# Performance work log

Hardware: AMD Instinct MI355X
Metric: run time of the kernel (lower is better)

## Reference

```python
import jax, jax.numpy as jnp
import numpy as np

N = 50000
E = 1600000
IN_C = 165
HID = 256
HEADS = 8
OUT_C = 2
NEG_SLOPE = 0.2


def setup_inputs() -> dict:
    key = jax.random.key(0)
    ks = jax.random.split(key, 10)
    x = jax.random.normal(ks[0], (N, IN_C), dtype=jnp.float32)
    edge_index = jax.random.randint(ks[1], (2, E), 0, N, dtype=jnp.int64)
    c1 = HID // HEADS  # 32 per-head channels in layer 1
    W1 = jax.random.normal(ks[2], (IN_C, HEADS * c1), dtype=jnp.float32) * (1.0 / np.sqrt(IN_C))
    att_src1 = jax.random.normal(ks[3], (HEADS, c1), dtype=jnp.float32) * 0.1
    att_dst1 = jax.random.normal(ks[4], (HEADS, c1), dtype=jnp.float32) * 0.1
    b1 = jnp.zeros((HEADS * c1,), dtype=jnp.float32)
    W2 = jax.random.normal(ks[5], (HID, 1 * OUT_C), dtype=jnp.float32) * (1.0 / np.sqrt(HID))
    att_src2 = jax.random.normal(ks[6], (1, OUT_C), dtype=jnp.float32) * 0.1
    att_dst2 = jax.random.normal(ks[7], (1, OUT_C), dtype=jnp.float32) * 0.1
    b2 = jnp.zeros((OUT_C,), dtype=jnp.float32)
    return {"x": x, "edge_index": edge_index, "W1": W1, "att_src1": att_src1,
            "att_dst1": att_dst1, "b1": b1, "W2": W2, "att_src2": att_src2,
            "att_dst2": att_dst2, "b2": b2}


def _gat_conv(x, src, dst, W, att_src, att_dst, bias, heads, concat):
    """PyG GATConv (eval mode, self-loops already appended to src/dst)."""
    n = x.shape[0]
    c = att_src.shape[1]
    h = (x @ W).reshape(n, heads, c)                      # [N, H, C]
    a_src = jnp.einsum('nhc,hc->nh', h, att_src)          # [N, H]
    a_dst = jnp.einsum('nhc,hc->nh', h, att_dst)
    e = a_src[src] + a_dst[dst]                           # [Et, H]
    e = jax.nn.leaky_relu(e, NEG_SLOPE)
    # segment softmax over incoming edges of each dst node
    e_max = jax.ops.segment_max(e, dst, num_segments=n)   # [N, H]
    e_exp = jnp.exp(e - e_max[dst])
    denom = jax.ops.segment_sum(e_exp, dst, num_segments=n)
    alpha = e_exp / denom[dst]                            # [Et, H]
    msg = alpha[:, :, None] * h[src]                      # [Et, H, C]
    out = jax.ops.segment_sum(msg, dst, num_segments=n)   # [N, H, C]
    if concat:
        out = out.reshape(n, heads * c)
    else:
        out = out.mean(axis=1)
    return out + bias


def reference(x, edge_index, W1, att_src1, att_dst1, b1, W2, att_src2, att_dst2, b2):
    n = x.shape[0]
    loops = jnp.arange(n, dtype=edge_index.dtype)
    src = jnp.concatenate([edge_index[0], loops])  # add_self_loops=True (PyG default)
    dst = jnp.concatenate([edge_index[1], loops])
    h = _gat_conv(x, src, dst, W1, att_src1, att_dst1, b1, HEADS, True)
    h = jax.nn.elu(h)
    out = _gat_conv(h, src, dst, W2, att_src2, att_dst2, b2, 1, False)
    return out
```

## Files before the change

### kernel.cpp

```cpp
#include <hip/hip_runtime.h>
#include <hip/hip_bf16.h>
#include <math.h>

#define N_NODES 50000
#define N_EDGES 1600000
#define IN_C 165
#define HID 256
#define HEADS 8
#define C1 32
#define OUT_C 2
#define NEG_SLOPE 0.2f
#define LOG2E 1.44269504088896f
#define TROWS 32
#define GEMM_BLOCKS ((N_NODES + TROWS - 1) / TROWS)
#define SCB 2048
#define SGRP 256
#define NPP ((N_NODES + 7) / 8)
#define CAPL 96
#define NE4 (N_EDGES / 4)

#define NSTEP 11
#define BIMG_BYTES ((size_t)NSTEP * 16384)
#define WAIMG_BYTES ((size_t)NSTEP * 2048)
#define WT (NSTEP * 512)
#define WPB ((WT + 255) / 256)
#define WAT (176 * 16)
#define WAB ((WAT + 255) / 256)

typedef float f32x2 __attribute__((ext_vector_type(2)));
typedef short s16x8 __attribute__((ext_vector_type(8)));
typedef float f32x16 __attribute__((ext_vector_type(16)));

__device__ inline float lrelu(float v) { return v > 0.f ? v : NEG_SLOPE * v; }
__device__ inline float e2l(float t) { return exp2f(fmaxf(t, NEG_SLOPE * t)); }

__device__ inline unsigned short f32_bf16(float f) {
    unsigned u = __float_as_uint(f);
    return (unsigned short)((u + 0x7FFFu + ((u >> 16) & 1u)) >> 16);
}

__device__ inline float bflo(unsigned u) { return __uint_as_float(u << 16); }
__device__ inline float bfhi(unsigned u) { return __uint_as_float(u & 0xFFFF0000u); }
__device__ inline float bf2f(unsigned short b) { return __uint_as_float(((unsigned)b) << 16); }

__global__ __launch_bounds__(256) void prep_kernel(
        const float* __restrict__ W,
        const float* __restrict__ att_src, const float* __restrict__ att_dst,
        unsigned short* __restrict__ bImg, unsigned short* __restrict__ waImg) {
    if (blockIdx.x < WPB) {
        int g2 = blockIdx.x * 256 + threadIdx.x;
        if (g2 >= WT) return;
        int s = g2 >> 9;
        int r9 = g2 & 511;
        int kg = r9 >> 8, nsub = (r9 >> 5) & 7, c32 = r9 & 31;
        int col = nsub * 32 + c32;
        int k0 = s * 16 + kg * 8;
        unsigned short hb[8], lb[8];
        #pragma unroll
        for (int i = 0; i < 8; ++i) {
            int k = k0 + i;
            float v = (k < IN_C) ? W[(size_t)k * HID + col] : 0.f;
            hb[i] = f32_bf16(v);
            lb[i] = f32_bf16(v - bf2f(hb[i]));
        }
        unsigned ph[4], pl[4];
        #pragma unroll
        for (int q = 0; q < 4; ++q) {
            ph[q] = (unsigned)hb[2*q] | ((unsigned)hb[2*q+1] << 16);
            pl[q] = (unsigned)lb[2*q] | ((unsigned)lb[2*q+1] << 16);
        }
        unsigned short* base = bImg + (size_t)s * 8192
                             + ((nsub * 2 + kg) * 32 + c32) * 8;
        *(uint4*)(base)        = make_uint4(ph[0], ph[1], ph[2], ph[3]);
        *(uint4*)(base + 4096) = make_uint4(pl[0], pl[1], pl[2], pl[3]);
    } else {
        int g2 = (blockIdx.x - WPB) * 256 + threadIdx.x;
        if (g2 >= WAT) return;
        int k = g2 >> 4, j = g2 & 15;
        int head = j >> 1;
        float dotv = 0.f;
        if (k < IN_C) {
            const float* wr = W + (size_t)k * HID + head * 32;
            const float* at = ((j & 1) ? att_dst : att_src) + head * 32;
            #pragma unroll
            for (int c = 0; c < 32; c += 4) {
                float4 wv = *(const float4*)(wr + c);
                float4 av = *(const float4*)(at + c);
                dotv += wv.x*av.x + wv.y*av.y + wv.z*av.z + wv.w*av.w;
            }
        }
        unsigned short dh = f32_bf16(dotv);
        unsigned short dl = f32_bf16(dotv - bf2f(dh));
        int s = k >> 4, kk = k & 15, kg = kk >> 3, i = kk & 7;
        unsigned short* base = waImg + (size_t)s * 1024 + (kg * 32 + j) * 8 + i;
        base[0]   = dh;
        base[512] = dl;
    }
}

__device__ __forceinline__ void gemm_mfma_block(
        int b, const float* __restrict__ x,
        const unsigned short* __restrict__ bImg,
        const unsigned short* __restrict__ waImg,
        unsigned short* __restrict__ h, float* __restrict__ a_src,
        float* __restrict__ a_dst, unsigned short* asr) {
    const int tid = threadIdx.x;
    const int w = tid >> 6, l = tid & 63;
    const int half = l >> 5, ln = l & 31;
    const int row0 = b * TROWS;
    for (int g = tid; g < 704; g += 256) {
        int o = g >> 5, row = g & 31;
        int s = o >> 1, kg = o & 1;
        int node = row0 + row;
        int k0 = o * 8;
        unsigned short hb[8], lb[8];
        #pragma unroll
        for (int i = 0; i < 8; ++i) {
            int k = k0 + i;
            float v = (node < N_NODES && k < IN_C) ? x[(size_t)node * IN_C + k] : 0.f;
            hb[i] = f32_bf16(v);
            lb[i] = f32_bf16(v - bf2f(hb[i]));
        }
        unsigned ph[4], pl[4];
        #pragma unroll
        for (int q = 0; q < 4; ++q) {
            ph[q] = (unsigned)hb[2*q] | ((unsigned)hb[2*q+1] << 16);
            pl[q] = (unsigned)lb[2*q] | ((unsigned)lb[2*q+1] << 16);
        }
        unsigned short* base = asr + s * 1024 + (kg * 32 + row) * 8;
        *(uint4*)(base)       = make_uint4(ph[0], ph[1], ph[2], ph[3]);
        *(uint4*)(base + 512) = make_uint4(pl[0], pl[1], pl[2], pl[3]);
    }
    __syncthreads();

    f32x16 acc0, acc1, accA;
    #pragma unroll
    for (int r = 0; r < 16; ++r) { acc0[r] = 0.f; acc1[r] = 0.f; accA[r] = 0.f; }
    const int ns0 = 2 * w, ns1 = 2 * w + 1;
    const int afo = (half * 32 + ln) * 8;
    const int fo0 = ((ns0 * 2 + half) * 32 + ln) * 8;
    const int fo1 = ((ns1 * 2 + half) * 32 + ln) * 8;
    for (int s = 0; s < NSTEP; ++s) {
        const unsigned short* ab = asr + s * 1024;
        s16x8 a_h = *(const s16x8*)(ab + afo);
        s16x8 a_l = *(const s16x8*)(ab + 512 + afo);
        const unsigned short* bb = bImg + (size_t)s * 8192;
        s16x8 bh0 = *(const s16x8*)(bb + fo0);
        s16x8 bh1 = *(const s16x8*)(bb + fo1);
        s16x8 bl0 = *(const s16x8*)(bb + 4096 + fo0);
        s16x8 bl1 = *(const s16x8*)(bb + 4096 + fo1);
        acc0 = __builtin_amdgcn_mfma_f32_32x32x16_bf16(a_h, bh0, acc0, 0, 0, 0);
        acc1 = __builtin_amdgcn_mfma_f32_32x32x16_bf16(a_h, bh1, acc1, 0, 0, 0);
        acc0 = __builtin_amdgcn_mfma_f32_32x32x16_bf16(a_h, bl0, acc0, 0, 0, 0);
        acc1 = __builtin_amdgcn_mfma_f32_32x32x16_bf16(a_h, bl1, acc1, 0, 0, 0);
        acc0 = __builtin_amdgcn_mfma_f32_32x32x16_bf16(a_l, bh0, acc0, 0, 0, 0);
        acc1 = __builtin_amdgcn_mfma_f32_32x32x16_bf16(a_l, bh1, acc1, 0, 0, 0);
        if (w == 0) {
            const unsigned short* wb = waImg + (size_t)s * 1024;
            s16x8 wah = *(const s16x8*)(wb + afo);
            s16x8 wal = *(const s16x8*)(wb + 512 + afo);
            accA = __builtin_amdgcn_mfma_f32_32x32x16_bf16(a_h, wah, accA, 0, 0, 0);
            accA = __builtin_amdgcn_mfma_f32_32x32x16_bf16(a_h, wal, accA, 0, 0, 0);
            accA = __builtin_amdgcn_mfma_f32_32x32x16_bf16(a_l, wah, accA, 0, 0, 0);
        }
    }
    #pragma unroll
    for (int t = 0; t < 2; ++t) {
        const int colg = w * 64 + t * 32 + ln;
        #pragma unroll
        for (int r = 0; r < 16; ++r) {
            int row = (r & 3) + 8 * (r >> 2) + 4 * half;
            int gr = row0 + row;
            if (gr < N_NODES) {
                float a = t ? acc1[r] : acc0[r];
                h[(size_t)gr * HID + colg] = f32_bf16(a);
            }
        }
    }
    if (w == 0 && ln < 16) {
        int head = ln >> 1;
        float* ap = (ln & 1) ? a_dst : a_src;
        #pragma unroll
        for (int r = 0; r < 16; ++r) {
            int row = (r & 3) + 8 * (r >> 2) + 4 * half;
            int gr = row0 + row;
            if (gr < N_NODES) ap[gr * 8 + head] = accA[r] * LOG2E;
        }
    }
}

__global__ __launch_bounds__(256) void fusedAB_kernel(
        const float* __restrict__ x,
        const unsigned short* __restrict__ bImg,
        const unsigned short* __restrict__ waImg,
        unsigned short* __restrict__ h, float* __restrict__ a_src,
        float* __restrict__ a_dst,
        const int* __restrict__ src, const int* __restrict__ dst,
        int* __restrict__ deg, unsigned short* __restrict__ csr) {
    __shared__ unsigned short asr[NSTEP * 1024];
    if (blockIdx.x < GEMM_BLOCKS) {
        gemm_mfma_block(blockIdx.x, x, bImg, waImg, h, a_src, a_dst, asr);
    } else {
        const int sb  = blockIdx.x - GEMM_BLOCKS;
        const int cls = sb & 7;
        const int blk = sb >> 3;
        const int lo = cls * NPP;
        const int hi = (lo + NPP < N_NODES) ? lo + NPP : N_NODES;
        const int t = blk * 256 + threadIdx.x;
        const int4* dst4 = (const int4*)dst;
        for (int uu = t; uu < NE4; uu += SGRP * 256) {
            int4 dv = dst4[uu];
            #pragma unroll
            for (int j = 0; j < 4; ++j) {
                int d = (j == 0) ? dv.x : (j == 1) ? dv.y : (j == 2) ? dv.z : dv.w;
                if (d >= lo && d < hi) {
                    int slot = atomicAdd(&deg[d], 1);
                    csr[(size_t)d * CAPL + slot] = (unsigned short)src[4 * uu + j];
                }
            }
        }
    }
}

__global__ __launch_bounds__(256) void agg1_fused_kernel(
        const int* __restrict__ deg, const unsigned short* __restrict__ csr,
        const float* __restrict__ a_src, const float* __restrict__ a_dst,
        const unsigned short* __restrict__ h1, const float* __restrict__ bias1,
        const float* __restrict__ W2,
        const float* __restrict__ as2, const float* __restrict__ ad2,
        float4* __restrict__ pk, float* __restrict__ a2d) {
    int wid = (blockIdx.x * 256 + threadIdx.x) >> 6;
    int l = threadIdx.x & 63;
    if (wid >= N_NODES) return;
    const int el = l >> 5;
    const int q  = l & 31;
    const int hd = q >> 2;
    const int ch = q * 8;
    const int sh = el * 16;
    const uint4* lst4 = (const uint4*)(csr + (size_t)wid * CAPL);
    const int n = deg[wid];
    const float ad_p = a_dst[wid * 8 + hd];
    float den = 0.f;
    f32x2 ac0 = {0.f, 0.f}, ac1 = {0.f, 0.f}, ac2 = {0.f, 0.f}, ac3 = {0.f, 0.f};

    uint4 ca = lst4[0], cb = lst4[1], cc = lst4[2], cd = lst4[3];
    int i = 0;

#define EXTRACT_S(S_, MK_, OFF_, W0_, W1_, W2_, W3_, W4_, W5_, W6_, W7_)      \
    {                                                                          \
        unsigned wsel_[8] = {W0_, W1_, W2_, W3_, W4_, W5_, W6_, W7_};          \
        _Pragma("unroll")                                                      \
        for (int j = 0; j < 8; ++j) {                                          \
            int sv = (int)((wsel_[j] >> sh) & 0xFFFFu);                        \
            int e = i + OFF_ + 2 * j + el;                                     \
            bool ok = e < n;                                                   \
            MK_[j] = ok ? 1.f : 0.f;                                           \
            S_[j] = ok ? sv : wid;                                             \
        }                                                                      \
    }

#define GATHER_ACC(S_, MK_, CNT_)                                              \
    {                                                                          \
        uint4 v_[CNT_];                                                        \
        _Pragma("unroll")                                                      \
        for (int j = 0; j < CNT_; ++j)                                         \
            v_[j] = *(const uint4*)(h1 + (size_t)S_[j] * HID + ch);            \
        float w_[CNT_];                                                        \
        _Pragma("unroll")                                                      \
        for (int j = 0; j < CNT_; ++j)                                         \
            w_[j] = MK_[j] * e2l(a_src[S_[j] * 8 + hd] + ad_p);                \
        _Pragma("unroll")                                                      \
        for (int j = 0; j < CNT_; ++j) {                                       \
            den += w_[j];                                                      \
            f32x2 w2_ = {w_[j], w_[j]};                                        \
            ac0 += w2_ * (f32x2){bflo(v_[j].x), bfhi(v_[j].x)};                \
            ac1 += w2_ * (f32x2){bflo(v_[j].y), bfhi(v_[j].y)};                \
            ac2 += w2_ * (f32x2){bflo(v_[j].z), bfhi(v_[j].z)};                \
            ac3 += w2_ * (f32x2){bflo(v_[j].w), bfhi(v_[j].w)};                \
        }                                                                      \
    }

    for (; i + 32 <= n; i += 32) {
        uint4 na = ca, nb = cb, nc = cc, nd = cd;
        if (i + 32 < n) {
            na = lst4[(i >> 3) + 4]; nb = lst4[(i >> 3) + 5];
            nc = lst4[(i >> 3) + 6]; nd = lst4[(i >> 3) + 7];
        }
        int s[16]; float mk[16];
        EXTRACT_S(s, mk, 0,  ca.x, ca.y, ca.z, ca.w, cb.x, cb.y, cb.z, cb.w)
        EXTRACT_S((s + 8), (mk + 8), 16, cc.x, cc.y, cc.z, cc.w, cd.x, cd.y, cd.z, cd.w)
        GATHER_ACC(s, mk, 16)
        ca = na; cb = nb; cc = nc; cd = nd;
    }
    if (i + 16 <= n) {
        int s[8]; float mk[8];
        EXTRACT_S(s, mk, 0, ca.x, ca.y, ca.z, ca.w, cb.x, cb.y, cb.z, cb.w)
        GATHER_ACC(s, mk, 8)
        ca = cc; cb = cd;
        i += 16;
    }
    if (i < n) {
        int s[8]; float mk[8];
        EXTRACT_S(s, mk, 0, ca.x, ca.y, ca.z, ca.w, cb.x, cb.y, cb.z, cb.w)
        GATHER_ACC(s, mk, 8)
    }
#undef EXTRACT_S
#undef GATHER_ACC

    float accs[8] = {ac0.x, ac0.y, ac1.x, ac1.y, ac2.x, ac2.y, ac3.x, ac3.y};
    den += __shfl_xor(den, 32);
    #pragma unroll
    for (int k = 0; k < 8; ++k) accs[k] += __shfl_xor(accs[k], 32);

    {
        float wsf = e2l(a_src[wid * 8 + hd] + ad_p);
        uint4 v = *(const uint4*)(h1 + (size_t)wid * HID + ch);
        den += wsf;
        accs[0] += wsf * bflo(v.x); accs[1] += wsf * bfhi(v.x);
        accs[2] += wsf * bflo(v.y); accs[3] += wsf * bfhi(v.y);
        accs[4] += wsf * bflo(v.z); accs[5] += wsf * bfhi(v.z);
        accs[6] += wsf * bflo(v.w); accs[7] += wsf * bfhi(v.w);
    }

    const float inv = 1.f / den;
    float4 bva = *(const float4*)(bias1 + ch);
    float4 bvb = *(const float4*)(bias1 + ch + 4);
    float o[8];
    o[0] = accs[0] * inv + bva.x; o[1] = accs[1] * inv + bva.y;
    o[2] = accs[2] * inv + bva.z; o[3] = accs[3] * inv + bva.w;
    o[4] = accs[4] * inv + bvb.x; o[5] = accs[5] * inv + bvb.y;
    o[6] = accs[6] * inv + bvb.z; o[7] = accs[7] * inv + bvb.w;
    #pragma unroll
    for (int k = 0; k < 8; ++k)
        o[k] = o[k] > 0.f ? o[k] : (__expf(o[k]) - 1.f);
    const float* wv = W2 + q * 16;
    float4 w0 = *(const float4*)(wv);
    float4 w1 = *(const float4*)(wv + 4);
    float4 w2 = *(const float4*)(wv + 8);
    float4 w3 = *(const float4*)(wv + 12);
    float p0 = o[0]*w0.x + o[1]*w0.z + o[2]*w1.x + o[3]*w1.z
             + o[4]*w2.x + o[5]*w2.z + o[6]*w3.x + o[7]*w3.z;
    float p1 = o[0]*w0.y + o[1]*w0.w + o[2]*w1.y + o[3]*w1.w
             + o[4]*w2.y + o[5]*w2.w + o[6]*w3.y + o[7]*w3.w;
    #pragma unroll
    for (int off = 16; off; off >>= 1) {
        p0 += __shfl_xor(p0, off);
        p1 += __shfl_xor(p1, off);
    }
    if (l == 0) {
        pk[wid] = make_float4(p0, p1, (p0 * as2[0] + p1 * as2[1]) * LOG2E, 0.f);
        a2d[wid] = (p0 * ad2[0] + p1 * ad2[1]) * LOG2E;
    }
}

__global__ __launch_bounds__(256) void agg2_fused_kernel(
        const int* __restrict__ deg, const unsigned short* __restrict__ csr,
        const float4* __restrict__ pk, const float* __restrict__ a2d,
        const float* __restrict__ b2, float* __restrict__ out) {
    int t = blockIdx.x * 256 + threadIdx.x;
    int node = t >> 4;
    int l = t & 15;
    if (node >= N_NODES) return;
    const unsigned short* lst = csr + (size_t)node * CAPL;
    const int n = deg[node];
    const float adv = a2d[node];
    float sm = 0.f, acc0 = 0.f, acc1 = 0.f;
    for (int i = l; i < n; i += 32) {
        int s0 = lst[i];
        int e1 = i + 16;
        bool ok1 = e1 < n;
        float m1 = ok1 ? 1.f : 0.f;
        int s1 = ok1 ? lst[e1] : node;
        float4 p0 = pk[s0], p1 = pk[s1];
        float w0 = e2l(p0.z + adv);
        float w1 = m1 * e2l(p1.z + adv);
        sm += w0 + w1;
        acc0 += w0 * p0.x + w1 * p1.x;
        acc1 += w0 * p0.y + w1 * p1.y;
    }
    #pragma unroll
    for (int off = 8; off; off >>= 1) {
        sm   += __shfl_xor(sm, off);
        acc0 += __shfl_xor(acc0, off);
        acc1 += __shfl_xor(acc1, off);
    }
    if (l == 0) {
        float4 ps = pk[node];
        float wsf = e2l(ps.z + adv);
        sm += wsf;
        acc0 += wsf * ps.x;
        acc1 += wsf * ps.y;
        *(float2*)(out + node * 2) =
            make_float2(acc0 / sm + b2[0], acc1 / sm + b2[1]);
    }
}

extern "C" void kernel_launch(void* const* d_in, const int* in_sizes, int n_in,
                              void* d_out, int out_size, void* d_ws, size_t ws_size,
                              hipStream_t stream) {
    (void)in_sizes; (void)n_in; (void)out_size; (void)ws_size;
    const float* x        = (const float*)d_in[0];
    const int*   ei       = (const int*)d_in[1];
    const float* W1       = (const float*)d_in[2];
    const float* att_src1 = (const float*)d_in[3];
    const float* att_dst1 = (const float*)d_in[4];
    const float* b1       = (const float*)d_in[5];
    const float* W2       = (const float*)d_in[6];
    const float* att_src2 = (const float*)d_in[7];
    const float* att_dst2 = (const float*)d_in[8];
    const float* b2       = (const float*)d_in[9];
    float* out = (float*)d_out;

    const int* src = ei;
    const int* dst = ei + N_EDGES;

    char* ws = (char*)d_ws;
    size_t off = 0;
    unsigned short* h1 = (unsigned short*)(ws + off);
    off += (size_t)N_NODES * HID * 2;
    float* a_src1 = (float*)(ws + off); off += (size_t)N_NODES * HEADS * 4;
    float* a_dst1 = (float*)(ws + off); off += (size_t)N_NODES * HEADS * 4;
    float4* pk = (float4*)(ws + off); off += (size_t)N_NODES * 16;
    float* a2d = (float*)(ws + off); off += (size_t)N_NODES * 4;
    int* deg    = (int*)(ws + off); off += (size_t)N_NODES * 4;
    unsigned short* csr = (unsigned short*)(ws + off);
    off += (size_t)N_NODES * CAPL * 2;
    unsigned short* bImg  = (unsigned short*)(ws + off); off += BIMG_BYTES;
    unsigned short* waImg = (unsigned short*)(ws + off); off += WAIMG_BYTES;

    hipMemsetAsync(deg, 0, (size_t)N_NODES * 4, stream);

    const int NW = (N_NODES * 64 + 255) / 256;

    prep_kernel<<<WPB + WAB, 256, 0, stream>>>(W1, att_src1, att_dst1, bImg, waImg);

    fusedAB_kernel<<<GEMM_BLOCKS + SCB, 256, 0, stream>>>(
        x, bImg, waImg, h1, a_src1, a_dst1, src, dst, deg, csr);

    agg1_fused_kernel<<<NW, 256, 0, stream>>>(
        deg, csr, a_src1, a_dst1, h1, b1, W2, att_src2, att_dst2, pk, a2d);

    agg2_fused_kernel<<<(N_NODES * 16 + 255) / 256, 256, 0, stream>>>(
        deg, csr, pk, a2d, b2, out);
}
```

Before: 319.0 us.

## Store layer-1 features head-major and aggregate per head in separate blocks

```diff
diff --git a/kernel.cpp b/kernel.cpp
--- a/kernel.cpp
+++ b/kernel.cpp
@@ -102,8 +102,8 @@
         int b, const float* __restrict__ x,
         const unsigned short* __restrict__ bImg,
         const unsigned short* __restrict__ waImg,
-        unsigned short* __restrict__ h, float* __restrict__ a_src,
-        float* __restrict__ a_dst, unsigned short* asr) {
+        unsigned short* __restrict__ h1h, float* __restrict__ a_srcH,
+        float* __restrict__ a_dstH, unsigned short* asr) {
     const int tid = threadIdx.x;
     const int w = tid >> 6, l = tid & 63;
     const int half = l >> 5, ln = l & 31;
@@ -166,25 +166,25 @@
     }
     #pragma unroll
     for (int t = 0; t < 2; ++t) {
-        const int colg = w * 64 + t * 32 + ln;
+        const int head = w * 2 + t;
         #pragma unroll
         for (int r = 0; r < 16; ++r) {
             int row = (r & 3) + 8 * (r >> 2) + 4 * half;
             int gr = row0 + row;
             if (gr < N_NODES) {
                 float a = t ? acc1[r] : acc0[r];
-                h[(size_t)gr * HID + colg] = f32_bf16(a);
+                h1h[((size_t)head * N_NODES + gr) * 32 + ln] = f32_bf16(a);
             }
         }
     }
     if (w == 0 && ln < 16) {
         int head = ln >> 1;
-        float* ap = (ln & 1) ? a_dst : a_src;
+        float* ap = (ln & 1) ? a_dstH : a_srcH;
         #pragma unroll
         for (int r = 0; r < 16; ++r) {
             int row = (r & 3) + 8 * (r >> 2) + 4 * half;
             int gr = row0 + row;
-            if (gr < N_NODES) ap[gr * 8 + head] = accA[r] * LOG2E;
+            if (gr < N_NODES) ap[(size_t)head * N_NODES + gr] = accA[r] * LOG2E;
         }
     }
 }
@@ -193,13 +193,13 @@
         const float* __restrict__ x,
         const unsigned short* __restrict__ bImg,
         const unsigned short* __restrict__ waImg,
-        unsigned short* __restrict__ h, float* __restrict__ a_src,
-        float* __restrict__ a_dst,
+        unsigned short* __restrict__ h1h, float* __restrict__ a_srcH,
+        float* __restrict__ a_dstH,
         const int* __restrict__ src, const int* __restrict__ dst,
         int* __restrict__ deg, unsigned short* __restrict__ csr) {
     __shared__ unsigned short asr[NSTEP * 1024];
     if (blockIdx.x < GEMM_BLOCKS) {
-        gemm_mfma_block(blockIdx.x, x, bImg, waImg, h, a_src, a_dst, asr);
+        gemm_mfma_block(blockIdx.x, x, bImg, waImg, h1h, a_srcH, a_dstH, asr);
     } else {
         const int sb  = blockIdx.x - GEMM_BLOCKS;
         const int cls = sb & 7;
@@ -222,135 +222,88 @@
     }
 }
 
-__global__ __launch_bounds__(256) void agg1_fused_kernel(
+__global__ __launch_bounds__(256) void agg1h_kernel(
         const int* __restrict__ deg, const unsigned short* __restrict__ csr,
-        const float* __restrict__ a_src, const float* __restrict__ a_dst,
-        const unsigned short* __restrict__ h1, const float* __restrict__ bias1,
-        const float* __restrict__ W2,
+        const float* __restrict__ a_srcH, const float* __restrict__ a_dstH,
+        const unsigned short* __restrict__ h1h, const float* __restrict__ bias1,
+        const float* __restrict__ W2, float* __restrict__ partial) {
+    const int h = blockIdx.x & 7;
+    const int node = (blockIdx.x >> 3) * 4 + (threadIdx.x >> 6);
+    if (node >= N_NODES) return;
+    const int l = threadIdx.x & 63;
+    const int eg = l >> 4;
+    const int c2 = l & 15;
+    const unsigned short* lst = csr + (size_t)node * CAPL;
+    const int n = __builtin_nontemporal_load(deg + node);
+    const float* asrc = a_srcH + (size_t)h * N_NODES;
+    const float ad_p = a_dstH[(size_t)h * N_NODES + node];
+    const unsigned short* hs = h1h + (size_t)h * N_NODES * 32;
+    float den = 0.f, ac0 = 0.f, ac1 = 0.f;
+    int i = 0;
+    for (; i + 8 <= n; i += 8) {
+        int s0 = __builtin_nontemporal_load(lst + i + eg);
+        int s1 = __builtin_nontemporal_load(lst + i + 4 + eg);
+        unsigned v0 = *(const unsigned*)(hs + (size_t)s0 * 32 + c2 * 2);
+        unsigned v1 = *(const unsigned*)(hs + (size_t)s1 * 32 + c2 * 2);
+        float w0 = e2l(asrc[s0] + ad_p);
+        float w1 = e2l(asrc[s1] + ad_p);
+        den += w0 + w1;
+        ac0 += w0 * bflo(v0) + w1 * bflo(v1);
+        ac1 += w0 * bfhi(v0) + w1 * bfhi(v1);
+    }
+    if (i < n) {
+        int e0 = i + eg, e1 = i + 4 + eg;
+        bool ok0 = e0 < n, ok1 = e1 < n;
+        int s0 = ok0 ? __builtin_nontemporal_load(lst + e0) : node;
+        int s1 = ok1 ? __builtin_nontemporal_load(lst + e1) : node;
+        unsigned v0 = *(const unsigned*)(hs + (size_t)s0 * 32 + c2 * 2);
+        unsigned v1 = *(const unsigned*)(hs + (size_t)s1 * 32 + c2 * 2);
+        float w0 = (ok0 ? 1.f : 0.f) * e2l(asrc[s0] + ad_p);
+        float w1 = (ok1 ? 1.f : 0.f) * e2l(asrc[s1] + ad_p);
+        den += w0 + w1;
+        ac0 += w0 * bflo(v0) + w1 * bflo(v1);
+        ac1 += w0 * bfhi(v0) + w1 * bfhi(v1);
+    }
+    den += __shfl_xor(den, 16); den += __shfl_xor(den, 32);
+    ac0 += __shfl_xor(ac0, 16); ac0 += __shfl_xor(ac0, 32);
+    ac1 += __shfl_xor(ac1, 16); ac1 += __shfl_xor(ac1, 32);
+    {
+        unsigned v = *(const unsigned*)(hs + (size_t)node * 32 + c2 * 2);
+        float ws = e2l(asrc[node] + ad_p);
+        den += ws;
+        ac0 += ws * bflo(v);
+        ac1 += ws * bfhi(v);
+    }
+    const float inv = 1.f / den;
+    float2 bv = *(const float2*)(bias1 + h * 32 + c2 * 2);
+    float o0 = ac0 * inv + bv.x;
+    float o1 = ac1 * inv + bv.y;
+    o0 = o0 > 0.f ? o0 : (__expf(o0) - 1.f);
+    o1 = o1 > 0.f ? o1 : (__expf(o1) - 1.f);
+    float4 wr = *(const float4*)(W2 + (h * 32 + c2 * 2) * 2);
+    float p0 = o0 * wr.x + o1 * wr.z;
+    float p1 = o0 * wr.y + o1 * wr.w;
+    #pragma unroll
+    for (int off = 1; off <= 8; off <<= 1) {
+        p0 += __shfl_xor(p0, off);
+        p1 += __shfl_xor(p1, off);
+    }
+    if (l == 0)
+        *(float2*)(partial + (size_t)node * 16 + h * 2) = make_float2(p0, p1);
+}
+
+__global__ __launch_bounds__(256) void fin_kernel(
+        const float* __restrict__ partial,
         const float* __restrict__ as2, const float* __restrict__ ad2,
         float4* __restrict__ pk, float* __restrict__ a2d) {
-    int wid = (blockIdx.x * 256 + threadIdx.x) >> 6;
-    int l = threadIdx.x & 63;
-    if (wid >= N_NODES) return;
-    const int el = l >> 5;
-    const int q  = l & 31;
-    const int hd = q >> 2;
-    const int ch = q * 8;
-    const int sh = el * 16;
-    const uint4* lst4 = (const uint4*)(csr + (size_t)wid * CAPL);
-    const int n = deg[wid];
-    const float ad_p = a_dst[wid * 8 + hd];
-    float den = 0.f;
-    f32x2 ac0 = {0.f, 0.f}, ac1 = {0.f, 0.f}, ac2 = {0.f, 0.f}, ac3 = {0.f, 0.f};
-
-    uint4 ca = lst4[0], cb = lst4[1], cc = lst4[2], cd = lst4[3];
-    int i = 0;
-
-#define EXTRACT_S(S_, MK_, OFF_, W0_, W1_, W2_, W3_, W4_, W5_, W6_, W7_)      \
-    {                                                                          \
-        unsigned wsel_[8] = {W0_, W1_, W2_, W3_, W4_, W5_, W6_, W7_};          \
-        _Pragma("unroll")                                                      \
-        for (int j = 0; j < 8; ++j) {                                          \
-            int sv = (int)((wsel_[j] >> sh) & 0xFFFFu);                        \
-            int e = i + OFF_ + 2 * j + el;                                     \
-            bool ok = e < n;                                                   \
-            MK_[j] = ok ? 1.f : 0.f;                                           \
-            S_[j] = ok ? sv : wid;                                             \
-        }                                                                      \
-    }
-
-#define GATHER_ACC(S_, MK_, CNT_)                                              \
-    {                                                                          \
-        uint4 v_[CNT_];                                                        \
-        _Pragma("unroll")                                                      \
-        for (int j = 0; j < CNT_; ++j)                                         \
-            v_[j] = *(const uint4*)(h1 + (size_t)S_[j] * HID + ch);            \
-        float w_[CNT_];                                                        \
-        _Pragma("unroll")                                                      \
-        for (int j = 0; j < CNT_; ++j)                                         \
-            w_[j] = MK_[j] * e2l(a_src[S_[j] * 8 + hd] + ad_p);                \
-        _Pragma("unroll")                                                      \
-        for (int j = 0; j < CNT_; ++j) {                                       \
-            den += w_[j];                                                      \
-            f32x2 w2_ = {w_[j], w_[j]};                                        \
-            ac0 += w2_ * (f32x2){bflo(v_[j].x), bfhi(v_[j].x)};                \
-            ac1 += w2_ * (f32x2){bflo(v_[j].y), bfhi(v_[j].y)};                \
-            ac2 += w2_ * (f32x2){bflo(v_[j].z), bfhi(v_[j].z)};                \
-            ac3 += w2_ * (f32x2){bflo(v_[j].w), bfhi(v_[j].w)};                \
-        }                                                                      \
-    }
-
-    for (; i + 32 <= n; i += 32) {
-        uint4 na = ca, nb = cb, nc = cc, nd = cd;
-        if (i + 32 < n) {
-            na = lst4[(i >> 3) + 4]; nb = lst4[(i >> 3) + 5];
-            nc = lst4[(i >> 3) + 6]; nd = lst4[(i >> 3) + 7];
-        }
-        int s[16]; float mk[16];
-        EXTRACT_S(s, mk, 0,  ca.x, ca.y, ca.z, ca.w, cb.x, cb.y, cb.z, cb.w)
-        EXTRACT_S((s + 8), (mk + 8), 16, cc.x, cc.y, cc.z, cc.w, cd.x, cd.y, cd.z, cd.w)
-        GATHER_ACC(s, mk, 16)
-        ca = na; cb = nb; cc = nc; cd = nd;
-    }
-    if (i + 16 <= n) {
-        int s[8]; float mk[8];
-        EXTRACT_S(s, mk, 0, ca.x, ca.y, ca.z, ca.w, cb.x, cb.y, cb.z, cb.w)
-        GATHER_ACC(s, mk, 8)
-        ca = cc; cb = cd;
-        i += 16;
-    }
-    if (i < n) {
-        int s[8]; float mk[8];
-        EXTRACT_S(s, mk, 0, ca.x, ca.y, ca.z, ca.w, cb.x, cb.y, cb.z, cb.w)
-        GATHER_ACC(s, mk, 8)
-    }
-#undef EXTRACT_S
-#undef GATHER_ACC
-
-    float accs[8] = {ac0.x, ac0.y, ac1.x, ac1.y, ac2.x, ac2.y, ac3.x, ac3.y};
-    den += __shfl_xor(den, 32);
-    #pragma unroll
-    for (int k = 0; k < 8; ++k) accs[k] += __shfl_xor(accs[k], 32);
-
-    {
-        float wsf = e2l(a_src[wid * 8 + hd] + ad_p);
-        uint4 v = *(const uint4*)(h1 + (size_t)wid * HID + ch);
-        den += wsf;
-        accs[0] += wsf * bflo(v.x); accs[1] += wsf * bfhi(v.x);
-        accs[2] += wsf * bflo(v.y); accs[3] += wsf * bfhi(v.y);
-        accs[4] += wsf * bflo(v.z); accs[5] += wsf * bfhi(v.z);
-        accs[6] += wsf * bflo(v.w); accs[7] += wsf * bfhi(v.w);
-    }
-
-    const float inv = 1.f / den;
-    float4 bva = *(const float4*)(bias1 + ch);
-    float4 bvb = *(const float4*)(bias1 + ch + 4);
-    float o[8];
-    o[0] = accs[0] * inv + bva.x; o[1] = accs[1] * inv + bva.y;
-    o[2] = accs[2] * inv + bva.z; o[3] = accs[3] * inv + bva.w;
-    o[4] = accs[4] * inv + bvb.x; o[5] = accs[5] * inv + bvb.y;
-    o[6] = accs[6] * inv + bvb.z; o[7] = accs[7] * inv + bvb.w;
-    #pragma unroll
-    for (int k = 0; k < 8; ++k)
-        o[k] = o[k] > 0.f ? o[k] : (__expf(o[k]) - 1.f);
-    const float* wv = W2 + q * 16;
-    float4 w0 = *(const float4*)(wv);
-    float4 w1 = *(const float4*)(wv + 4);
-    float4 w2 = *(const float4*)(wv + 8);
-    float4 w3 = *(const float4*)(wv + 12);
-    float p0 = o[0]*w0.x + o[1]*w0.z + o[2]*w1.x + o[3]*w1.z
-             + o[4]*w2.x + o[5]*w2.z + o[6]*w3.x + o[7]*w3.z;
-    float p1 = o[0]*w0.y + o[1]*w0.w + o[2]*w1.y + o[3]*w1.w
-             + o[4]*w2.y + o[5]*w2.w + o[6]*w3.y + o[7]*w3.w;
-    #pragma unroll
-    for (int off = 16; off; off >>= 1) {
-        p0 += __shfl_xor(p0, off);
-        p1 += __shfl_xor(p1, off);
-    }
-    if (l == 0) {
-        pk[wid] = make_float4(p0, p1, (p0 * as2[0] + p1 * as2[1]) * LOG2E, 0.f);
-        a2d[wid] = (p0 * ad2[0] + p1 * ad2[1]) * LOG2E;
-    }
+    int node = blockIdx.x * 256 + threadIdx.x;
+    if (node >= N_NODES) return;
+    const float4* pp = (const float4*)(partial + (size_t)node * 16);
+    float4 q0 = pp[0], q1 = pp[1], q2 = pp[2], q3 = pp[3];
+    float p0 = q0.x + q0.z + q1.x + q1.z + q2.x + q2.z + q3.x + q3.z;
+    float p1 = q0.y + q0.w + q1.y + q1.w + q2.y + q2.w + q3.y + q3.w;
+    pk[node] = make_float4(p0, p1, (p0 * as2[0] + p1 * as2[1]) * LOG2E, 0.f);
+    a2d[node] = (p0 * ad2[0] + p1 * ad2[1]) * LOG2E;
 }
 
 __global__ __launch_bounds__(256) void agg2_fused_kernel(
@@ -416,29 +369,31 @@
 
     char* ws = (char*)d_ws;
     size_t off = 0;
-    unsigned short* h1 = (unsigned short*)(ws + off);
+    unsigned short* h1h = (unsigned short*)(ws + off);
     off += (size_t)N_NODES * HID * 2;
-    float* a_src1 = (float*)(ws + off); off += (size_t)N_NODES * HEADS * 4;
-    float* a_dst1 = (float*)(ws + off); off += (size_t)N_NODES * HEADS * 4;
+    float* a_srcH = (float*)(ws + off); off += (size_t)N_NODES * HEADS * 4;
+    float* a_dstH = (float*)(ws + off); off += (size_t)N_NODES * HEADS * 4;
     float4* pk = (float4*)(ws + off); off += (size_t)N_NODES * 16;
     float* a2d = (float*)(ws + off); off += (size_t)N_NODES * 4;
     int* deg    = (int*)(ws + off); off += (size_t)N_NODES * 4;
     unsigned short* csr = (unsigned short*)(ws + off);
     off += (size_t)N_NODES * CAPL * 2;
+    float* partial = (float*)(ws + off); off += (size_t)N_NODES * 16 * 4;
     unsigned short* bImg  = (unsigned short*)(ws + off); off += BIMG_BYTES;
     unsigned short* waImg = (unsigned short*)(ws + off); off += WAIMG_BYTES;
 
     hipMemsetAsync(deg, 0, (size_t)N_NODES * 4, stream);
 
-    const int NW = (N_NODES * 64 + 255) / 256;
-
     prep_kernel<<<WPB + WAB, 256, 0, stream>>>(W1, att_src1, att_dst1, bImg, waImg);
 
     fusedAB_kernel<<<GEMM_BLOCKS + SCB, 256, 0, stream>>>(
-        x, bImg, waImg, h1, a_src1, a_dst1, src, dst, deg, csr);
-
-    agg1_fused_kernel<<<NW, 256, 0, stream>>>(
-        deg, csr, a_src1, a_dst1, h1, b1, W2, att_src2, att_dst2, pk, a2d);
+        x, bImg, waImg, h1h, a_srcH, a_dstH, src, dst, deg, csr);
+
+    agg1h_kernel<<<(N_NODES / 4) * 8, 256, 0, stream>>>(
+        deg, csr, a_srcH, a_dstH, h1h, b1, W2, partial);
+
+    fin_kernel<<<(N_NODES + 255) / 256, 256, 0, stream>>>(
+        partial, att_src2, att_dst2, pk, a2d);
 
     agg2_fused_kernel<<<(N_NODES * 16 + 255) / 256, 256, 0, stream>>>(
         deg, csr, pk, a2d, b2, out);
```

New measurement: 492.9 us. 54.5% more time.
